# Kernel optimization log

Hardware: AMD Instinct MI355X
Metric: run time of the kernel (lower is better)

## Reference

```python
import jax, jax.numpy as jnp
import numpy as np

B, T, D = 2, 2048, 2048
H, HD = 16, 128
ROPE_BASE = 10000.0
EPS = 1e-6


def setup_inputs() -> dict:
    key = jax.random.key(0)
    ks = jax.random.split(key, 5)
    s = 1.0 / np.sqrt(D)
    return {
        "x": jax.random.normal(ks[0], (B, T, D), dtype=jnp.float32),
        "Wq": jax.random.normal(ks[1], (H * HD, D), dtype=jnp.float32) * s,
        "Wk": jax.random.normal(ks[2], (H * HD, D), dtype=jnp.float32) * s,
        "Wv": jax.random.normal(ks[3], (H * HD, D), dtype=jnp.float32) * s,
        "Wo": jax.random.normal(ks[4], (D, H * HD), dtype=jnp.float32) * s,
        "q_norm_w": jnp.ones((HD,), dtype=jnp.float32),
        "k_norm_w": jnp.ones((HD,), dtype=jnp.float32),
    }


def _rms_norm(x, w):
    # RMSNorm over last dim, no centering (LLaMA/Qwen style)
    norm = jnp.sqrt(jnp.mean(jnp.square(x), axis=-1, keepdims=True) + EPS)
    return x / norm * w


def _rope_interleaved(x):
    # x: (B, T, H, HD); GPT-NeoX interleaved style, sequential positions
    dim = HD // 2
    freqs = jnp.exp(-jnp.arange(0, dim, dtype=jnp.float32) * jnp.log(ROPE_BASE) / dim)
    angles = jnp.arange(T, dtype=jnp.float32)[:, None] * freqs[None, :]  # (T, dim)
    cos = jnp.cos(angles)[None, :, None, :]  # (1, T, 1, dim)
    sin = jnp.sin(angles)[None, :, None, :]
    x_even = x[..., ::2]
    x_odd = x[..., 1::2]
    r_even = x_even * cos - x_odd * sin
    r_odd = x_even * sin + x_odd * cos
    return jnp.stack([r_even, r_odd], axis=-1).reshape(x.shape)


def reference(x, Wq, Wk, Wv, Wo, q_norm_w, k_norm_w):
    # QKV projections (weights stored [out, in], per llm_linear einsum)
    q = jnp.einsum("btd,od->bto", x, Wq).reshape(B, T, H, HD)
    k = jnp.einsum("btd,od->bto", x, Wk).reshape(B, T, H, HD)
    v = jnp.einsum("btd,od->bto", x, Wv).reshape(B, T, H, HD)
    # per-head QK RMSNorm
    q = _rms_norm(q, q_norm_w)
    k = _rms_norm(k, k_norm_w)
    # rotary embeddings
    q = _rope_interleaved(q)
    k = _rope_interleaved(k)
    # causal scaled dot-product attention
    scale = 1.0 / jnp.sqrt(jnp.asarray(HD, dtype=x.dtype))
    scores = jnp.einsum("bthd,bshd->bhts", q, k) * scale  # (B, H, T, T)
    causal = jnp.tril(jnp.ones((T, T), dtype=bool))
    scores = jnp.where(causal[None, None, :, :], scores, jnp.asarray(-1e30, dtype=scores.dtype))
    probs = jax.nn.softmax(scores, axis=-1)
    ctx = jnp.einsum("bhts,bshd->bthd", probs, v).reshape(B, T, H * HD)
    # output projection
    return jnp.einsum("bto,do->btd", ctx, Wo)
```

## Files before the change

### kernel.cpp

```cpp
#include <hip/hip_runtime.h>
#include <cstdint>
#include <cstddef>

#define B_ 2
#define T_ 2048
#define D_ 2048
#define H_ 16
#define HD_ 128
#define EPS_ 1e-6f
#define QSCALE_ 0.08838834764831845f
#define KVSTRIDE_ (H_ * HD_)

typedef unsigned short u16;
typedef short s16x8 __attribute__((ext_vector_type(8)));
typedef float f32x4 __attribute__((ext_vector_type(4)));

__device__ __forceinline__ float bf2f(u16 h) {
  union { unsigned int u; float f; } v;
  v.u = ((unsigned int)h) << 16;
  return v.f;
}
__device__ __forceinline__ u16 f2bf(float f) {
  union { float f; unsigned int u; } v;
  v.f = f;
  unsigned int r = v.u + 0x7FFFu + ((v.u >> 16) & 1u);
  return (u16)(r >> 16);
}

__device__ __forceinline__ void gload16(const void* g, void* l) {
  __builtin_amdgcn_global_load_lds(
      (const __attribute__((address_space(1))) unsigned int*)g,
      (__attribute__((address_space(3))) unsigned int*)l, 16, 0, 0);
}

__global__ void cvt_f32_bf16(const float* __restrict__ in, u16* __restrict__ out, int n4) {
  int i = blockIdx.x * blockDim.x + threadIdx.x;
  if (i < n4) {
    float4 v = ((const float4*)in)[i];
    ((ushort4*)out)[i] = make_ushort4(f2bf(v.x), f2bf(v.y), f2bf(v.z), f2bf(v.w));
  }
}

template <int OUT_BF16>
__global__ __launch_bounds__(256, 2) void gemm_btn(const u16* __restrict__ A,
                                                   const u16* __restrict__ Bm,
                                                   void* __restrict__ Cout,
                                                   int M, int N, int K) {
  __shared__ u16 As[128 * 32];
  __shared__ u16 Bs[128 * 32];
  const int tid = threadIdx.x;
  const int w = tid >> 6, lane = tid & 63, quad = lane >> 4, c = lane & 15;
  const int wm = w & 1, wn = w >> 1;
  const int m0 = blockIdx.y * 128, n0 = blockIdx.x * 128;

  f32x4 acc[4][4];
#pragma unroll
  for (int i = 0; i < 4; ++i)
#pragma unroll
    for (int j = 0; j < 4; ++j) acc[i][j] = (f32x4){0.f, 0.f, 0.f, 0.f};

  for (int k0 = 0; k0 < K; k0 += 32) {
    __syncthreads();
#pragma unroll
    for (int i = 0; i < 2; ++i) {
      int chunk = (w * 2 + i) * 64 + lane;
      int row = chunk >> 2, cc = chunk & 3;
      gload16(A + (size_t)(m0 + row) * K + k0 + cc * 8, (void*)(As + chunk * 8));
      gload16(Bm + (size_t)(n0 + row) * K + k0 + cc * 8, (void*)(Bs + chunk * 8));
    }
    __syncthreads();
    s16x8 af[4], bf[4];
#pragma unroll
    for (int mi = 0; mi < 4; ++mi)
      af[mi] = *(const s16x8*)(As + (wm * 64 + mi * 16 + c) * 32 + quad * 8);
#pragma unroll
    for (int ni = 0; ni < 4; ++ni)
      bf[ni] = *(const s16x8*)(Bs + (wn * 64 + ni * 16 + c) * 32 + quad * 8);
#pragma unroll
    for (int mi = 0; mi < 4; ++mi)
#pragma unroll
      for (int ni = 0; ni < 4; ++ni)
        acc[mi][ni] = __builtin_amdgcn_mfma_f32_16x16x32_bf16(af[mi], bf[ni], acc[mi][ni], 0, 0, 0);
  }

#pragma unroll
  for (int mi = 0; mi < 4; ++mi)
#pragma unroll
    for (int ni = 0; ni < 4; ++ni)
#pragma unroll
      for (int r = 0; r < 4; ++r) {
        int row = m0 + wm * 64 + mi * 16 + quad * 4 + r;
        int col = n0 + wn * 64 + ni * 16 + c;
        float v = acc[mi][ni][r];
        if (OUT_BF16)
          ((u16*)Cout)[(size_t)row * N + col] = f2bf(v);
        else
          ((float*)Cout)[(size_t)row * N + col] = v;
      }
}

__global__ void rmsnorm_rope(u16* __restrict__ x, const float* __restrict__ nw, float outscale) {
  const int tid = threadIdx.x;
  const int w = tid >> 6, lane = tid & 63;
  const int vec = blockIdx.x * 4 + w;
  const int t = (vec >> 4) & (T_ - 1);
  u16* base = x + (size_t)vec * HD_;
  unsigned int pk = *(const unsigned int*)(base + lane * 2);
  float e = bf2f((u16)(pk & 0xFFFFu));
  float o = bf2f((u16)(pk >> 16));
  float ss = e * e + o * o;
#pragma unroll
  for (int off = 1; off < 64; off <<= 1) ss += __shfl_xor(ss, off, 64);
  float rn = rsqrtf(ss * (1.0f / HD_) + EPS_);
  float we = nw[lane * 2], wo = nw[lane * 2 + 1];
  e = e * rn * we;
  o = o * rn * wo;
  float freq = expf(-(float)lane * (9.210340371976184f / 64.0f));
  float ang = (float)t * freq;
  float sn, cs;
  sincosf(ang, &sn, &cs);
  float re = (e * cs - o * sn) * outscale;
  float ro = (e * sn + o * cs) * outscale;
  *(unsigned int*)(base + lane * 2) = ((unsigned int)f2bf(ro) << 16) | (unsigned int)f2bf(re);
}

__global__ __launch_bounds__(256, 2) void attn_fwd(const u16* __restrict__ Q,
                                                   const u16* __restrict__ Kg,
                                                   const u16* __restrict__ Vt,
                                                   u16* __restrict__ O) {
  __shared__ u16 Ks[64 * 136];
  __shared__ u16 Vts[128 * 72];
  __shared__ u16 Ps[64 * 72];
  const int tid = threadIdx.x;
  const int w = tid >> 6, lane = tid & 63, quad = lane >> 4, c = lane & 15;
  const int bid = blockIdx.x;
  const int qt = 31 - (bid >> 5);
  const int h = bid & 15;
  const int b = (bid >> 4) & 1;
  const int q0 = qt * 64;

  s16x8 qf[4];
  const u16* qbase = Q + ((size_t)(b * T_ + q0 + w * 16 + c) * H_ + h) * HD_;
#pragma unroll
  for (int kk = 0; kk < 4; ++kk) qf[kk] = *(const s16x8*)(qbase + kk * 32 + quad * 8);

  f32x4 of[8];
#pragma unroll
  for (int i = 0; i < 8; ++i) of[i] = (f32x4){0.f, 0.f, 0.f, 0.f};
  float m_i[4] = {-1e30f, -1e30f, -1e30f, -1e30f};
  float l_i[4] = {0.f, 0.f, 0.f, 0.f};

  const u16* kbase = Kg + ((size_t)b * T_ * H_ + h) * HD_;
  const u16* vtbase = Vt + (size_t)(h * HD_) * (B_ * T_) + b * T_;

  for (int j = 0; j <= qt; ++j) {
    __syncthreads();
    const u16* krow = kbase + (size_t)(j * 64) * KVSTRIDE_;
    const u16* vrow = vtbase + j * 64;
#pragma unroll
    for (int i = 0; i < 4; ++i) {
      int chunk = i * 256 + tid;
      int krowi = chunk >> 4, kc = chunk & 15;
      *(uint4*)(&Ks[krowi * 136 + kc * 8]) =
          *(const uint4*)(krow + (size_t)krowi * KVSTRIDE_ + kc * 8);
      int vrowi = chunk >> 3, vc = chunk & 7;
      *(uint4*)(&Vts[vrowi * 72 + vc * 8]) =
          *(const uint4*)(vrow + (size_t)vrowi * (B_ * T_) + vc * 8);
    }
    __syncthreads();

    f32x4 sf[4];
#pragma unroll
    for (int ni = 0; ni < 4; ++ni) {
      f32x4 a = (f32x4){0.f, 0.f, 0.f, 0.f};
#pragma unroll
      for (int kk = 0; kk < 4; ++kk) {
        s16x8 bfr = *(const s16x8*)(&Ks[(ni * 16 + c) * 136 + kk * 32 + quad * 8]);
        a = __builtin_amdgcn_mfma_f32_16x16x32_bf16(qf[kk], bfr, a, 0, 0, 0);
      }
      sf[ni] = a;
    }
    if (j == qt) {
#pragma unroll
      for (int ni = 0; ni < 4; ++ni)
#pragma unroll
        for (int r = 0; r < 4; ++r) {
          int rowg = w * 16 + quad * 4 + r;
          int colg = ni * 16 + c;
          if (colg > rowg) sf[ni][r] = -1e30f;
        }
    }
    float mc[4];
#pragma unroll
    for (int r = 0; r < 4; ++r)
      mc[r] = fmaxf(fmaxf(sf[0][r], sf[1][r]), fmaxf(sf[2][r], sf[3][r]));
#pragma unroll
    for (int off = 1; off < 16; off <<= 1)
#pragma unroll
      for (int r = 0; r < 4; ++r) mc[r] = fmaxf(mc[r], __shfl_xor(mc[r], off, 64));
#pragma unroll
    for (int r = 0; r < 4; ++r) {
      float mnew = fmaxf(m_i[r], mc[r]);
      float alpha = __expf(m_i[r] - mnew);
      m_i[r] = mnew;
      l_i[r] *= alpha;
#pragma unroll
      for (int ot = 0; ot < 8; ++ot) of[ot][r] *= alpha;
    }
    float rs[4] = {0.f, 0.f, 0.f, 0.f};
#pragma unroll
    for (int ni = 0; ni < 4; ++ni)
#pragma unroll
      for (int r = 0; r < 4; ++r) {
        float p = __expf(sf[ni][r] - m_i[r]);
        sf[ni][r] = p;
        rs[r] += p;
      }
#pragma unroll
    for (int off = 1; off < 16; off <<= 1)
#pragma unroll
      for (int r = 0; r < 4; ++r) rs[r] += __shfl_xor(rs[r], off, 64);
#pragma unroll
    for (int r = 0; r < 4; ++r) l_i[r] += rs[r];
#pragma unroll
    for (int ni = 0; ni < 4; ++ni)
#pragma unroll
      for (int r = 0; r < 4; ++r)
        Ps[(w * 16 + quad * 4 + r) * 72 + ni * 16 + c] = f2bf(sf[ni][r]);
    __syncthreads();
    s16x8 pa[2];
    pa[0] = *(const s16x8*)(&Ps[(w * 16 + c) * 72 + quad * 8]);
    pa[1] = *(const s16x8*)(&Ps[(w * 16 + c) * 72 + 32 + quad * 8]);
#pragma unroll
    for (int ot = 0; ot < 8; ++ot) {
#pragma unroll
      for (int kk = 0; kk < 2; ++kk) {
        s16x8 vfr = *(const s16x8*)(&Vts[(ot * 16 + c) * 72 + kk * 32 + quad * 8]);
        of[ot] = __builtin_amdgcn_mfma_f32_16x16x32_bf16(pa[kk], vfr, of[ot], 0, 0, 0);
      }
    }
  }

  float inv[4];
#pragma unroll
  for (int r = 0; r < 4; ++r) inv[r] = 1.0f / l_i[r];
  u16* obase = O + ((size_t)(b * T_ + q0) * H_ + h) * HD_;
#pragma unroll
  for (int ot = 0; ot < 8; ++ot)
#pragma unroll
    for (int r = 0; r < 4; ++r)
      obase[(size_t)(w * 16 + quad * 4 + r) * KVSTRIDE_ + ot * 16 + c] = f2bf(of[ot][r] * inv[r]);
}

extern "C" void kernel_launch(void* const* d_in, const int* in_sizes, int n_in,
                              void* d_out, int out_size, void* d_ws, size_t ws_size,
                              hipStream_t stream) {
  const float* x = (const float*)d_in[0];
  const float* Wq = (const float*)d_in[1];
  const float* Wk = (const float*)d_in[2];
  const float* Wv = (const float*)d_in[3];
  const float* Wo = (const float*)d_in[4];
  const float* qw = (const float*)d_in[5];
  const float* kw = (const float*)d_in[6];
  float* out = (float*)d_out;

  const size_t xE = (size_t)B_ * T_ * D_;
  const size_t wE = (size_t)D_ * H_ * HD_;
  const size_t need = xE * 2 * 5 + wE * 2 * 4;
  if (ws_size < need) return;

  char* ws = (char*)d_ws;
  u16* xb = (u16*)ws;   ws += xE * 2;
  u16* wqb = (u16*)ws;  ws += wE * 2;
  u16* wkb = (u16*)ws;  ws += wE * 2;
  u16* wvb = (u16*)ws;  ws += wE * 2;
  u16* wob = (u16*)ws;  ws += wE * 2;
  u16* qb = (u16*)ws;   ws += xE * 2;
  u16* kb = (u16*)ws;   ws += xE * 2;
  u16* vtb = (u16*)ws;  ws += xE * 2;
  u16* ctxb = (u16*)ws; ws += xE * 2;

  cvt_f32_bf16<<<xE / 1024, 256, 0, stream>>>(x, xb, (int)(xE / 4));
  cvt_f32_bf16<<<wE / 1024, 256, 0, stream>>>(Wq, wqb, (int)(wE / 4));
  cvt_f32_bf16<<<wE / 1024, 256, 0, stream>>>(Wk, wkb, (int)(wE / 4));
  cvt_f32_bf16<<<wE / 1024, 256, 0, stream>>>(Wv, wvb, (int)(wE / 4));
  cvt_f32_bf16<<<wE / 1024, 256, 0, stream>>>(Wo, wob, (int)(wE / 4));

  dim3 gg(16, 32);
  gemm_btn<1><<<gg, 256, 0, stream>>>(xb, wqb, qb, 4096, 2048, 2048);
  gemm_btn<1><<<gg, 256, 0, stream>>>(xb, wkb, kb, 4096, 2048, 2048);
  dim3 ggv(32, 16);
  gemm_btn<1><<<ggv, 256, 0, stream>>>(wvb, xb, vtb, 2048, 4096, 2048);

  rmsnorm_rope<<<16384, 256, 0, stream>>>(qb, qw, QSCALE_);
  rmsnorm_rope<<<16384, 256, 0, stream>>>(kb, kw, 1.0f);

  attn_fwd<<<B_ * H_ * (T_ / 64), 256, 0, stream>>>(qb, kb, vtb, ctxb);

  gemm_btn<0><<<gg, 256, 0, stream>>>(ctxb, wob, out, 4096, 2048, 2048);
}
```

Baseline: 447.5 us.

## Use 128-row query tiles in attention and batch projection, norm and convert launches

The attention kernel now gives each block 128 query rows, two 16-row MFMA tiles per wave, so each K/V tile loaded into LDS is reused twice as much. K/V tiles are staged with global_load_lds into XOR-swizzled, unpadded LDS, and one barrier per iteration is dropped. Query blocks are ordered so heavy and light causal tiles are interleaved across the grid. Separately, the five conversion launches, three QKV GEMMs and two RMSNorm/RoPE passes are each merged into one launch. The trade-offs are higher register pressure, with the occupancy hint removed, and half of the QKV GEMM blocks that exit immediately.

```diff
diff --git a/kernel.cpp b/kernel.cpp
--- a/kernel.cpp
+++ b/kernel.cpp
@@ -33,18 +33,96 @@
       (__attribute__((address_space(3))) unsigned int*)l, 16, 0, 0);
 }
 
-__global__ void cvt_f32_bf16(const float* __restrict__ in, u16* __restrict__ out, int n4) {
-  int i = blockIdx.x * blockDim.x + threadIdx.x;
-  if (i < n4) {
-    float4 v = ((const float4*)in)[i];
-    ((ushort4*)out)[i] = make_ushort4(f2bf(v.x), f2bf(v.y), f2bf(v.z), f2bf(v.w));
-  }
-}
-
-template <int OUT_BF16>
-__global__ __launch_bounds__(256, 2) void gemm_btn(const u16* __restrict__ A,
+__global__ void cvt_all(const float* __restrict__ x, const float* __restrict__ wq,
+                        const float* __restrict__ wk, const float* __restrict__ wv,
+                        const float* __restrict__ wo, u16* __restrict__ xb,
+                        u16* __restrict__ wqb, u16* __restrict__ wkb,
+                        u16* __restrict__ wvb, u16* __restrict__ wob) {
+  int bid = blockIdx.x;
+  const float* in;
+  u16* out;
+  int i;
+  if (bid < 8192) {
+    in = x; out = xb; i = bid * 256 + threadIdx.x;
+  } else {
+    int r = (bid - 8192) >> 12;
+    int wb = (bid - 8192) & 4095;
+    const float* ins[4] = {wq, wk, wv, wo};
+    u16* outs[4] = {wqb, wkb, wvb, wob};
+    in = ins[r]; out = outs[r]; i = wb * 256 + threadIdx.x;
+  }
+  float4 v = ((const float4*)in)[i];
+  ((ushort4*)out)[i] = make_ushort4(f2bf(v.x), f2bf(v.y), f2bf(v.z), f2bf(v.w));
+}
+
+__global__ __launch_bounds__(256, 2) void gemm_qkv(const u16* __restrict__ xb,
+                                                   const u16* __restrict__ wq,
+                                                   const u16* __restrict__ wk,
+                                                   const u16* __restrict__ wv,
+                                                   u16* __restrict__ qo,
+                                                   u16* __restrict__ ko,
+                                                   u16* __restrict__ vo) {
+  const u16 *A, *Bm;
+  u16* C;
+  int M, N;
+  if (blockIdx.z == 0)      { A = xb; Bm = wq; C = qo; M = 4096; N = 2048; }
+  else if (blockIdx.z == 1) { A = xb; Bm = wk; C = ko; M = 4096; N = 2048; }
+  else                      { A = wv; Bm = xb; C = vo; M = 2048; N = 4096; }
+  const int m0 = blockIdx.y * 128, n0 = blockIdx.x * 128;
+  if (m0 >= M || n0 >= N) return;
+  const int K = 2048;
+
+  __shared__ u16 As[128 * 32];
+  __shared__ u16 Bs[128 * 32];
+  const int tid = threadIdx.x;
+  const int w = tid >> 6, lane = tid & 63, quad = lane >> 4, c = lane & 15;
+  const int wm = w & 1, wn = w >> 1;
+
+  f32x4 acc[4][4];
+#pragma unroll
+  for (int i = 0; i < 4; ++i)
+#pragma unroll
+    for (int j = 0; j < 4; ++j) acc[i][j] = (f32x4){0.f, 0.f, 0.f, 0.f};
+
+  for (int k0 = 0; k0 < K; k0 += 32) {
+    __syncthreads();
+#pragma unroll
+    for (int i = 0; i < 2; ++i) {
+      int chunk = (w * 2 + i) * 64 + lane;
+      int row = chunk >> 2, cc = chunk & 3;
+      gload16(A + (size_t)(m0 + row) * K + k0 + cc * 8, (void*)(As + chunk * 8));
+      gload16(Bm + (size_t)(n0 + row) * K + k0 + cc * 8, (void*)(Bs + chunk * 8));
+    }
+    __syncthreads();
+    s16x8 af[4], bf[4];
+#pragma unroll
+    for (int mi = 0; mi < 4; ++mi)
+      af[mi] = *(const s16x8*)(As + (wm * 64 + mi * 16 + c) * 32 + quad * 8);
+#pragma unroll
+    for (int ni = 0; ni < 4; ++ni)
+      bf[ni] = *(const s16x8*)(Bs + (wn * 64 + ni * 16 + c) * 32 + quad * 8);
+#pragma unroll
+    for (int mi = 0; mi < 4; ++mi)
+#pragma unroll
+      for (int ni = 0; ni < 4; ++ni)
+        acc[mi][ni] = __builtin_amdgcn_mfma_f32_16x16x32_bf16(af[mi], bf[ni], acc[mi][ni], 0, 0, 0);
+  }
+
+#pragma unroll
+  for (int mi = 0; mi < 4; ++mi)
+#pragma unroll
+    for (int ni = 0; ni < 4; ++ni)
+#pragma unroll
+      for (int r = 0; r < 4; ++r) {
+        int row = m0 + wm * 64 + mi * 16 + quad * 4 + r;
+        int col = n0 + wn * 64 + ni * 16 + c;
+        C[(size_t)row * N + col] = f2bf(acc[mi][ni][r]);
+      }
+}
+
+__global__ __launch_bounds__(256, 2) void gemm_out(const u16* __restrict__ A,
                                                    const u16* __restrict__ Bm,
-                                                   void* __restrict__ Cout,
+                                                   float* __restrict__ Cout,
                                                    int M, int N, int K) {
   __shared__ u16 As[128 * 32];
   __shared__ u16 Bs[128 * 32];
@@ -91,15 +169,15 @@
       for (int r = 0; r < 4; ++r) {
         int row = m0 + wm * 64 + mi * 16 + quad * 4 + r;
         int col = n0 + wn * 64 + ni * 16 + c;
-        float v = acc[mi][ni][r];
-        if (OUT_BF16)
-          ((u16*)Cout)[(size_t)row * N + col] = f2bf(v);
-        else
-          ((float*)Cout)[(size_t)row * N + col] = v;
+        Cout[(size_t)row * N + col] = acc[mi][ni][r];
       }
 }
 
-__global__ void rmsnorm_rope(u16* __restrict__ x, const float* __restrict__ nw, float outscale) {
+__global__ void rmsnorm_rope2(u16* __restrict__ qx, u16* __restrict__ kx,
+                              const float* __restrict__ qw, const float* __restrict__ kw) {
+  u16* x = blockIdx.y ? kx : qx;
+  const float* nw = blockIdx.y ? kw : qw;
+  const float outscale = blockIdx.y ? 1.0f : QSCALE_;
   const int tid = threadIdx.x;
   const int w = tid >> 6, lane = tid & 63;
   const int vec = blockIdx.x * 4 + w;
@@ -124,132 +202,162 @@
   *(unsigned int*)(base + lane * 2) = ((unsigned int)f2bf(ro) << 16) | (unsigned int)f2bf(re);
 }
 
-__global__ __launch_bounds__(256, 2) void attn_fwd(const u16* __restrict__ Q,
-                                                   const u16* __restrict__ Kg,
-                                                   const u16* __restrict__ Vt,
-                                                   u16* __restrict__ O) {
-  __shared__ u16 Ks[64 * 136];
-  __shared__ u16 Vts[128 * 72];
-  __shared__ u16 Ps[64 * 72];
+__global__ __launch_bounds__(256) void attn_fwd(const u16* __restrict__ Q,
+                                                const u16* __restrict__ Kg,
+                                                const u16* __restrict__ Vt,
+                                                u16* __restrict__ O) {
+  __shared__ u16 Ks[64 * 128];
+  __shared__ u16 Vts[128 * 64];
+  __shared__ u16 Ps[128 * 72];
   const int tid = threadIdx.x;
   const int w = tid >> 6, lane = tid & 63, quad = lane >> 4, c = lane & 15;
   const int bid = blockIdx.x;
-  const int qt = 31 - (bid >> 5);
-  const int h = bid & 15;
-  const int b = (bid >> 4) & 1;
-  const int q0 = qt * 64;
-
-  s16x8 qf[4];
-  const u16* qbase = Q + ((size_t)(b * T_ + q0 + w * 16 + c) * H_ + h) * HD_;
-#pragma unroll
-  for (int kk = 0; kk < 4; ++kk) qf[kk] = *(const s16x8*)(qbase + kk * 32 + quad * 8);
-
-  f32x4 of[8];
-#pragma unroll
-  for (int i = 0; i < 8; ++i) of[i] = (f32x4){0.f, 0.f, 0.f, 0.f};
-  float m_i[4] = {-1e30f, -1e30f, -1e30f, -1e30f};
-  float l_i[4] = {0.f, 0.f, 0.f, 0.f};
+  int qb, hb;
+  if (bid < 256) { qb = 15 - ((bid >> 5) & 7); hb = bid & 31; }
+  else           { qb = (bid >> 5) & 7;        hb = bid & 31; }
+  const int h = hb & 15, b = hb >> 4;
+  const int q0 = qb * 128;
+  const int jmax = 2 * qb + 1;
+
+  s16x8 qf[2][4];
+#pragma unroll
+  for (int mi = 0; mi < 2; ++mi) {
+    const u16* qbase = Q + ((size_t)(b * T_ + q0 + w * 32 + mi * 16 + c) * H_ + h) * HD_;
+#pragma unroll
+    for (int kk = 0; kk < 4; ++kk) qf[mi][kk] = *(const s16x8*)(qbase + kk * 32 + quad * 8);
+  }
+
+  f32x4 of[2][8];
+#pragma unroll
+  for (int mi = 0; mi < 2; ++mi)
+#pragma unroll
+    for (int ot = 0; ot < 8; ++ot) of[mi][ot] = (f32x4){0.f, 0.f, 0.f, 0.f};
+  float m_i[2][4], l_i[2][4];
+#pragma unroll
+  for (int mi = 0; mi < 2; ++mi)
+#pragma unroll
+    for (int r = 0; r < 4; ++r) { m_i[mi][r] = -1e30f; l_i[mi][r] = 0.f; }
 
   const u16* kbase = Kg + ((size_t)b * T_ * H_ + h) * HD_;
-  const u16* vtbase = Vt + (size_t)(h * HD_) * (B_ * T_) + b * T_;
-
-  for (int j = 0; j <= qt; ++j) {
+  const u16* vtbase = Vt + (size_t)(h * HD_) * (B_ * T_) + (size_t)b * T_;
+
+  for (int j = 0; j <= jmax; ++j) {
     __syncthreads();
     const u16* krow = kbase + (size_t)(j * 64) * KVSTRIDE_;
     const u16* vrow = vtbase + j * 64;
 #pragma unroll
     for (int i = 0; i < 4; ++i) {
       int chunk = i * 256 + tid;
-      int krowi = chunk >> 4, kc = chunk & 15;
-      *(uint4*)(&Ks[krowi * 136 + kc * 8]) =
-          *(const uint4*)(krow + (size_t)krowi * KVSTRIDE_ + kc * 8);
-      int vrowi = chunk >> 3, vc = chunk & 7;
-      *(uint4*)(&Vts[vrowi * 72 + vc * 8]) =
-          *(const uint4*)(vrow + (size_t)vrowi * (B_ * T_) + vc * 8);
-    }
-    __syncthreads();
-
-    f32x4 sf[4];
+      int kr = chunk >> 4, kc = chunk & 15;
+      gload16(krow + (size_t)kr * KVSTRIDE_ + (size_t)((kc ^ (kr & 7)) * 8),
+              (void*)(Ks + chunk * 8));
+      int vr = chunk >> 3, vc = chunk & 7;
+      gload16(vrow + (size_t)vr * (B_ * T_) + (size_t)((vc ^ (vr & 7)) * 8),
+              (void*)(Vts + chunk * 8));
+    }
+    __syncthreads();
+
+    f32x4 sf[2][4];
 #pragma unroll
     for (int ni = 0; ni < 4; ++ni) {
-      f32x4 a = (f32x4){0.f, 0.f, 0.f, 0.f};
-#pragma unroll
-      for (int kk = 0; kk < 4; ++kk) {
-        s16x8 bfr = *(const s16x8*)(&Ks[(ni * 16 + c) * 136 + kk * 32 + quad * 8]);
-        a = __builtin_amdgcn_mfma_f32_16x16x32_bf16(qf[kk], bfr, a, 0, 0, 0);
+      s16x8 kf[4];
+#pragma unroll
+      for (int kk = 0; kk < 4; ++kk)
+        kf[kk] = *(const s16x8*)(Ks + (ni * 16 + c) * 128 + (((kk * 4 + quad) ^ (c & 7)) * 8));
+#pragma unroll
+      for (int mi = 0; mi < 2; ++mi) {
+        f32x4 a = (f32x4){0.f, 0.f, 0.f, 0.f};
+#pragma unroll
+        for (int kk = 0; kk < 4; ++kk)
+          a = __builtin_amdgcn_mfma_f32_16x16x32_bf16(qf[mi][kk], kf[kk], a, 0, 0, 0);
+        sf[mi][ni] = a;
       }
-      sf[ni] = a;
-    }
-    if (j == qt) {
+    }
+    if ((j + 1) * 64 > q0 + w * 32) {
+#pragma unroll
+      for (int mi = 0; mi < 2; ++mi)
+#pragma unroll
+        for (int ni = 0; ni < 4; ++ni)
+#pragma unroll
+          for (int r = 0; r < 4; ++r) {
+            int rowg = q0 + w * 32 + mi * 16 + quad * 4 + r;
+            int colg = j * 64 + ni * 16 + c;
+            if (colg > rowg) sf[mi][ni][r] = -1e30f;
+          }
+    }
+#pragma unroll
+    for (int mi = 0; mi < 2; ++mi) {
+      float mc[4];
+#pragma unroll
+      for (int r = 0; r < 4; ++r)
+        mc[r] = fmaxf(fmaxf(sf[mi][0][r], sf[mi][1][r]), fmaxf(sf[mi][2][r], sf[mi][3][r]));
+#pragma unroll
+      for (int off = 1; off < 16; off <<= 1)
+#pragma unroll
+        for (int r = 0; r < 4; ++r) mc[r] = fmaxf(mc[r], __shfl_xor(mc[r], off, 64));
+#pragma unroll
+      for (int r = 0; r < 4; ++r) {
+        float mnew = fmaxf(m_i[mi][r], mc[r]);
+        float alpha = __expf(m_i[mi][r] - mnew);
+        m_i[mi][r] = mnew;
+        l_i[mi][r] *= alpha;
+#pragma unroll
+        for (int ot = 0; ot < 8; ++ot) of[mi][ot][r] *= alpha;
+      }
+      float rs[4] = {0.f, 0.f, 0.f, 0.f};
 #pragma unroll
       for (int ni = 0; ni < 4; ++ni)
 #pragma unroll
         for (int r = 0; r < 4; ++r) {
-          int rowg = w * 16 + quad * 4 + r;
-          int colg = ni * 16 + c;
-          if (colg > rowg) sf[ni][r] = -1e30f;
+          float p = __expf(sf[mi][ni][r] - m_i[mi][r]);
+          sf[mi][ni][r] = p;
+          rs[r] += p;
         }
-    }
-    float mc[4];
-#pragma unroll
-    for (int r = 0; r < 4; ++r)
-      mc[r] = fmaxf(fmaxf(sf[0][r], sf[1][r]), fmaxf(sf[2][r], sf[3][r]));
-#pragma unroll
-    for (int off = 1; off < 16; off <<= 1)
-#pragma unroll
-      for (int r = 0; r < 4; ++r) mc[r] = fmaxf(mc[r], __shfl_xor(mc[r], off, 64));
-#pragma unroll
-    for (int r = 0; r < 4; ++r) {
-      float mnew = fmaxf(m_i[r], mc[r]);
-      float alpha = __expf(m_i[r] - mnew);
-      m_i[r] = mnew;
-      l_i[r] *= alpha;
-#pragma unroll
-      for (int ot = 0; ot < 8; ++ot) of[ot][r] *= alpha;
-    }
-    float rs[4] = {0.f, 0.f, 0.f, 0.f};
-#pragma unroll
-    for (int ni = 0; ni < 4; ++ni)
-#pragma unroll
-      for (int r = 0; r < 4; ++r) {
-        float p = __expf(sf[ni][r] - m_i[r]);
-        sf[ni][r] = p;
-        rs[r] += p;
-      }
-#pragma unroll
-    for (int off = 1; off < 16; off <<= 1)
-#pragma unroll
-      for (int r = 0; r < 4; ++r) rs[r] += __shfl_xor(rs[r], off, 64);
-#pragma unroll
-    for (int r = 0; r < 4; ++r) l_i[r] += rs[r];
-#pragma unroll
-    for (int ni = 0; ni < 4; ++ni)
+#pragma unroll
+      for (int off = 1; off < 16; off <<= 1)
+#pragma unroll
+        for (int r = 0; r < 4; ++r) rs[r] += __shfl_xor(rs[r], off, 64);
+#pragma unroll
+      for (int r = 0; r < 4; ++r) l_i[mi][r] += rs[r];
+#pragma unroll
+      for (int ni = 0; ni < 4; ++ni)
+#pragma unroll
+        for (int r = 0; r < 4; ++r)
+          Ps[(w * 32 + mi * 16 + quad * 4 + r) * 72 + ni * 16 + c] = f2bf(sf[mi][ni][r]);
+    }
+    s16x8 pa[2][2];
+#pragma unroll
+    for (int mi = 0; mi < 2; ++mi)
+#pragma unroll
+      for (int kk = 0; kk < 2; ++kk)
+        pa[mi][kk] = *(const s16x8*)(Ps + (w * 32 + mi * 16 + c) * 72 + kk * 32 + quad * 8);
+#pragma unroll
+    for (int ot = 0; ot < 8; ++ot) {
+      s16x8 vf[2];
+#pragma unroll
+      for (int kk = 0; kk < 2; ++kk)
+        vf[kk] = *(const s16x8*)(Vts + (ot * 16 + c) * 64 + (((kk * 4 + quad) ^ (c & 7)) * 8));
+#pragma unroll
+      for (int mi = 0; mi < 2; ++mi)
+#pragma unroll
+        for (int kk = 0; kk < 2; ++kk)
+          of[mi][ot] = __builtin_amdgcn_mfma_f32_16x16x32_bf16(pa[mi][kk], vf[kk], of[mi][ot], 0, 0, 0);
+    }
+  }
+
+  u16* obase = O + ((size_t)(b * T_ + q0 + w * 32) * H_ + h) * HD_;
+#pragma unroll
+  for (int mi = 0; mi < 2; ++mi) {
+    float inv[4];
+#pragma unroll
+    for (int r = 0; r < 4; ++r) inv[r] = 1.0f / l_i[mi][r];
+#pragma unroll
+    for (int ot = 0; ot < 8; ++ot)
 #pragma unroll
       for (int r = 0; r < 4; ++r)
-        Ps[(w * 16 + quad * 4 + r) * 72 + ni * 16 + c] = f2bf(sf[ni][r]);
-    __syncthreads();
-    s16x8 pa[2];
-    pa[0] = *(const s16x8*)(&Ps[(w * 16 + c) * 72 + quad * 8]);
-    pa[1] = *(const s16x8*)(&Ps[(w * 16 + c) * 72 + 32 + quad * 8]);
-#pragma unroll
-    for (int ot = 0; ot < 8; ++ot) {
-#pragma unroll
-      for (int kk = 0; kk < 2; ++kk) {
-        s16x8 vfr = *(const s16x8*)(&Vts[(ot * 16 + c) * 72 + kk * 32 + quad * 8]);
-        of[ot] = __builtin_amdgcn_mfma_f32_16x16x32_bf16(pa[kk], vfr, of[ot], 0, 0, 0);
-      }
-    }
-  }
-
-  float inv[4];
-#pragma unroll
-  for (int r = 0; r < 4; ++r) inv[r] = 1.0f / l_i[r];
-  u16* obase = O + ((size_t)(b * T_ + q0) * H_ + h) * HD_;
-#pragma unroll
-  for (int ot = 0; ot < 8; ++ot)
-#pragma unroll
-    for (int r = 0; r < 4; ++r)
-      obase[(size_t)(w * 16 + quad * 4 + r) * KVSTRIDE_ + ot * 16 + c] = f2bf(of[ot][r] * inv[r]);
+        obase[(size_t)(mi * 16 + quad * 4 + r) * KVSTRIDE_ + ot * 16 + c] =
+            f2bf(of[mi][ot][r] * inv[r]);
+  }
 }
 
 extern "C" void kernel_launch(void* const* d_in, const int* in_sizes, int n_in,
@@ -280,22 +388,13 @@
   u16* vtb = (u16*)ws;  ws += xE * 2;
   u16* ctxb = (u16*)ws; ws += xE * 2;
 
-  cvt_f32_bf16<<<xE / 1024, 256, 0, stream>>>(x, xb, (int)(xE / 4));
-  cvt_f32_bf16<<<wE / 1024, 256, 0, stream>>>(Wq, wqb, (int)(wE / 4));
-  cvt_f32_bf16<<<wE / 1024, 256, 0, stream>>>(Wk, wkb, (int)(wE / 4));
-  cvt_f32_bf16<<<wE / 1024, 256, 0, stream>>>(Wv, wvb, (int)(wE / 4));
-  cvt_f32_bf16<<<wE / 1024, 256, 0, stream>>>(Wo, wob, (int)(wE / 4));
-
-  dim3 gg(16, 32);
-  gemm_btn<1><<<gg, 256, 0, stream>>>(xb, wqb, qb, 4096, 2048, 2048);
-  gemm_btn<1><<<gg, 256, 0, stream>>>(xb, wkb, kb, 4096, 2048, 2048);
-  dim3 ggv(32, 16);
-  gemm_btn<1><<<ggv, 256, 0, stream>>>(wvb, xb, vtb, 2048, 4096, 2048);
-
-  rmsnorm_rope<<<16384, 256, 0, stream>>>(qb, qw, QSCALE_);
-  rmsnorm_rope<<<16384, 256, 0, stream>>>(kb, kw, 1.0f);
-
-  attn_fwd<<<B_ * H_ * (T_ / 64), 256, 0, stream>>>(qb, kb, vtb, ctxb);
-
-  gemm_btn<0><<<gg, 256, 0, stream>>>(ctxb, wob, out, 4096, 2048, 2048);
-}
+  cvt_all<<<8192 + 4 * 4096, 256, 0, stream>>>(x, Wq, Wk, Wv, Wo, xb, wqb, wkb, wvb, wob);
+
+  gemm_qkv<<<dim3(32, 32, 3), 256, 0, stream>>>(xb, wqb, wkb, wvb, qb, kb, vtb);
+
+  rmsnorm_rope2<<<dim3(16384, 2), 256, 0, stream>>>(qb, kb, qw, kw);
+
+  attn_fwd<<<512, 256, 0, stream>>>(qb, kb, vtb, ctxb);
+
+  gemm_out<<<dim3(16, 32), 256, 0, stream>>>(ctxb, wob, out, 4096, 2048, 2048);
+}
```

Result: slower. 517.6 us (+15.7%).
